# Performance work log

Measured on AMD Instinct MI355X. Metric: run time of the kernel, lower is better.

The kernel has to match this reference:

```python
import jax, jax.numpy as jnp
import numpy as np

WH, WW = 7, 7          # window size
S0, S1 = 3, 3          # shift size
NH = 12                # num heads
C = 384                # channels


def _rel_pos_index(wh, ww):
    coords = np.stack(np.meshgrid(np.arange(wh), np.arange(ww), indexing='ij')).reshape(2, -1)
    rel = coords[:, :, None] - coords[:, None, :]          # [2, N, N]
    rel = rel.transpose(1, 2, 0).astype(np.int64)          # [N, N, 2]
    rel[..., 0] += wh - 1
    rel[..., 1] += ww - 1
    rel[..., 0] *= 2 * ww - 1
    return rel.sum(-1)                                      # [N, N]


def _shift_mask(ph, pw, wh, ww, s0, s1):
    img = np.zeros((ph, pw), dtype=np.float32)
    cnt = 0
    for hs in ((0, ph - wh), (ph - wh, ph - s0), (ph - s0, ph)):
        for ws in ((0, pw - ww), (pw - ww, pw - s1), (pw - s1, pw)):
            img[hs[0]:hs[1], ws[0]:ws[1]] = cnt
            cnt += 1
    win = img.reshape(ph // wh, wh, pw // ww, ww).transpose(0, 2, 1, 3).reshape(-1, wh * ww)
    diff = win[:, None, :] - win[:, :, None]               # [nW, N, N]
    return np.where(diff != 0, -100.0, 0.0).astype(np.float32)


def setup_inputs() -> dict:
    key = jax.random.key(0)
    ks = jax.random.split(key, 6)
    return {
        'x': jax.random.normal(ks[0], (32, 56, 56, C), jnp.float32),
        'qkv_w': jax.random.normal(ks[1], (3 * C, C), jnp.float32) * 0.02,
        'qkv_b': jax.random.normal(ks[2], (3 * C,), jnp.float32) * 0.02,
        'proj_w': jax.random.normal(ks[3], (C, C), jnp.float32) * 0.02,
        'proj_b': jax.random.normal(ks[4], (C,), jnp.float32) * 0.02,
        'rpb_table': jax.random.normal(ks[5], ((2 * WH - 1) * (2 * WW - 1), NH), jnp.float32) * 0.02,
    }


def reference(x, qkv_w, qkv_b, proj_w, proj_b, rpb_table):
    b, h, w, c = x.shape
    pad_b, pad_r = (-h) % WH, (-w) % WW
    x = jnp.pad(x, ((0, 0), (0, pad_b), (0, pad_r), (0, 0)))
    ph, pw = h + pad_b, w + pad_r
    s0 = 0 if WH >= ph else S0
    s1 = 0 if WW >= pw else S1
    if s0 + s1 > 0:
        x = jnp.roll(x, (-s0, -s1), axis=(1, 2))
    nwh, nww = ph // WH, pw // WW
    nw = nwh * nww
    N = WH * WW
    hd = c // NH
    # window partition -> [b*nw, N, c]
    xw = x.reshape(b, nwh, WH, nww, WW, c).transpose(0, 1, 3, 2, 4, 5).reshape(b * nw, N, c)
    qkv = xw @ qkv_w.T + qkv_b
    qkv = qkv.reshape(b * nw, N, 3, NH, hd).transpose(2, 0, 3, 1, 4)  # [3, B_, H, N, hd]
    q, k, v = qkv[0] * (hd ** -0.5), qkv[1], qkv[2]
    attn = jnp.einsum('bhnd,bhmd->bhnm', q, k)                        # [B_, H, N, N]
    rel_idx = _rel_pos_index(WH, WW)
    bias = rpb_table[rel_idx.reshape(-1)].reshape(N, N, NH).transpose(2, 0, 1)
    attn = attn + bias[None]
    if s0 + s1 > 0:
        mask = jnp.asarray(_shift_mask(ph, pw, WH, WW, s0, s1))        # [nw, N, N]
        attn = attn.reshape(b, nw, NH, N, N) + mask[None, :, None]
        attn = attn.reshape(b * nw, NH, N, N)
    attn = jax.nn.softmax(attn, axis=-1)
    out = jnp.einsum('bhnm,bhmd->bhnd', attn, v).transpose(0, 2, 1, 3).reshape(b * nw, N, c)
    out = out @ proj_w.T + proj_b
    # window reverse -> [b, ph, pw, c]
    out = out.reshape(b, nwh, nww, WH, WW, c).transpose(0, 1, 3, 2, 4, 5).reshape(b, ph, pw, c)
    if s0 + s1 > 0:
        out = jnp.roll(out, (s0, s1), axis=(1, 2))
    return out[:, :h, :w, :]
```

## Files before the change

### kernel.cpp

```cpp
#include <hip/hip_runtime.h>
#include <hip/hip_bf16.h>
#include <stdint.h>


typedef __bf16 v8bf __attribute__((ext_vector_type(8)));
typedef __bf16 v4bf __attribute__((ext_vector_type(4)));
typedef float  v4f  __attribute__((ext_vector_type(4)));

#define MFMA16(a,b,c) __builtin_amdgcn_mfma_f32_16x16x32_bf16(a,b,c,0,0,0)

typedef const void __attribute__((address_space(1))) gas_t;
typedef void __attribute__((address_space(3))) las_t;

__device__ __forceinline__ void gl2lds16(const void* g, void* l) {
  __builtin_amdgcn_global_load_lds((gas_t*)g, (las_t*)l, 16, 0, 0);
}

__global__ __launch_bounds__(256) void gather_cvt_x(const float* __restrict__ x,
                                                    __bf16* __restrict__ xw) {
  uint32_t cid = blockIdx.x * 256u + threadIdx.x;
  uint32_t m   = cid / 96u, c4 = cid - (cid / 96u) * 96u;
  uint32_t win = m / 49u,  tok = m - win * 49u;
  uint32_t b  = win >> 6,  wy = (win >> 3) & 7u, wx = win & 7u;
  uint32_t ty = tok / 7u,  tx = tok - ty * 7u;
  uint32_t sy = wy * 7u + ty + 3u; if (sy >= 56u) sy -= 56u;
  uint32_t sx = wx * 7u + tx + 3u; if (sx >= 56u) sx -= 56u;
  const float4 v = *(const float4*)(x + (((size_t)(b * 56u + sy)) * 56u + sx) * 384u + c4 * 4u);
  v4bf o; o[0] = (__bf16)v.x; o[1] = (__bf16)v.y; o[2] = (__bf16)v.z; o[3] = (__bf16)v.w;
  *(v4bf*)(xw + (size_t)m * 384u + c4 * 4u) = o;
}

__global__ __launch_bounds__(256) void cvt_w_kernel(const float* __restrict__ qw,
                                                    const float* __restrict__ pw,
                                                    __bf16* __restrict__ dq,
                                                    __bf16* __restrict__ dp) {
  uint32_t cid = blockIdx.x * 256u + threadIdx.x;
  uint32_t e = cid * 4u;
  const float* src; __bf16* dst; uint32_t off;
  if (e < 442368u) { src = qw; dst = dq; off = e; }
  else             { src = pw; dst = dp; off = e - 442368u; }
  float4 v = *(const float4*)(src + off);
  v4bf o; o[0] = (__bf16)v.x; o[1] = (__bf16)v.y; o[2] = (__bf16)v.z; o[3] = (__bf16)v.w;
  *(v4bf*)(dst + off) = o;
}

template<int EPI>
__global__ __launch_bounds__(256) void gemm_bt(const __bf16* __restrict__ A,
                                               const __bf16* __restrict__ B,
                                               const float* __restrict__ biasv,
                                               __bf16* __restrict__ Qp,
                                               __bf16* __restrict__ Kp,
                                               __bf16* __restrict__ Vp,
                                               float* __restrict__ Op) {
  __shared__ __bf16 lds_a[128 * 32];
  __shared__ __bf16 lds_b[128 * 32];
  const int tid = threadIdx.x, wv = tid >> 6, ln = tid & 63;
  const int wr = wv >> 1, wc = wv & 1;
  const int c = ln & 15, rq = (ln >> 4) * 4;
  const uint32_t m0 = blockIdx.y * 128u, n0 = blockIdx.x * 128u;
  v4f acc[4][4] = {};
  for (int ks = 0; ks < 12; ++ks) {
    const uint32_t k0 = ks * 32u;
    for (int ch = wv; ch < 8; ch += 4) {
      uint32_t e = ch * 512u + (uint32_t)ln * 8u;
      uint32_t row = e >> 5, col = e & 31u;
      gl2lds16(A + (size_t)(m0 + row) * 384u + k0 + col, lds_a + ch * 512);
      gl2lds16(B + (size_t)(n0 + row) * 384u + k0 + col, lds_b + ch * 512);
    }
    __syncthreads();
    const __bf16* pa = lds_a + (wr * 64 + c) * 32 + rq * 2;
    const __bf16* pb = lds_b + (wc * 64 + c) * 32 + rq * 2;
    v8bf af[4], bfr[4];
#pragma unroll
    for (int i = 0; i < 4; ++i) af[i]  = *(const v8bf*)(pa + i * 16 * 32);
#pragma unroll
    for (int i = 0; i < 4; ++i) bfr[i] = *(const v8bf*)(pb + i * 16 * 32);
#pragma unroll
    for (int mi = 0; mi < 4; ++mi)
#pragma unroll
      for (int ni = 0; ni < 4; ++ni)
        acc[mi][ni] = MFMA16(af[mi], bfr[ni], acc[mi][ni]);
    __syncthreads();
  }

  if (EPI == 0) {
    const uint32_t which = blockIdx.x / 3u;
    __bf16* dst = (which == 0u) ? Qp : (which == 1u) ? Kp : Vp;
    const float scl = (which == 0u) ? 0.17677669529663687f : 1.0f;
#pragma unroll
    for (int ni = 0; ni < 4; ++ni) {
      uint32_t colg = n0 + wc * 64u + ni * 16u + c;
      float bv = biasv[colg];
      uint32_t cw = colg - which * 384u;
      uint32_t head = cw >> 5, d = cw & 31u;
#pragma unroll
      for (int mi = 0; mi < 4; ++mi)
#pragma unroll
        for (int r = 0; r < 4; ++r) {
          uint32_t mg = m0 + wr * 64u + mi * 16u + rq + r;
          uint32_t win = mg / 49u, tok = mg - win * 49u;
          float val = (acc[mi][ni][r] + bv) * scl;
          dst[((size_t)(win * 12u + head) * 49u + tok) * 32u + d] = (__bf16)val;
        }
    }
  } else {
#pragma unroll
    for (int ni = 0; ni < 4; ++ni) {
      uint32_t colg = n0 + wc * 64u + ni * 16u + c;
      float bv = biasv[colg];
#pragma unroll
      for (int mi = 0; mi < 4; ++mi)
#pragma unroll
        for (int r = 0; r < 4; ++r) {
          uint32_t mg = m0 + wr * 64u + mi * 16u + rq + r;
          uint32_t win = mg / 49u, tok = mg - win * 49u;
          uint32_t b = win >> 6, wy = (win >> 3) & 7u, wx = win & 7u;
          uint32_t ty = tok / 7u, tx = tok - ty * 7u;
          uint32_t y = wy * 7u + ty + 3u; if (y >= 56u) y -= 56u;
          uint32_t x = wx * 7u + tx + 3u; if (x >= 56u) x -= 56u;
          Op[(((size_t)b * 56u + y) * 56u + x) * 384u + colg] = acc[mi][ni][r] + bv;
        }
    }
  }
}

__global__ __launch_bounds__(256) void attn_kernel(const __bf16* __restrict__ Q,
                                                   const __bf16* __restrict__ K,
                                                   const __bf16* __restrict__ V,
                                                   const float* __restrict__ rpb,
                                                   __bf16* __restrict__ Oa) {
  __shared__ __bf16 plds[4][64 * 72];
  const int tid = threadIdx.x, wv = tid >> 6, ln = tid & 63;
  const int c = ln & 15, rq = (ln >> 4) * 4;
  const uint32_t gwh = blockIdx.x * 4u + wv;
  const uint32_t win = gwh / 12u, head = gwh - win * 12u;
  const uint32_t wy = (win >> 3) & 7u, wx = win & 7u;
  const __bf16* qb = Q + (size_t)gwh * 1568u;
  const __bf16* kb = K + (size_t)gwh * 1568u;
  const __bf16* vb = V + (size_t)gwh * 1568u;

  v8bf qf[4], kf[4];
#pragma unroll
  for (int t = 0; t < 4; ++t) {
    qf[t] = *(const v8bf*)(qb + (t * 16 + c) * 32 + rq * 2);
    kf[t] = *(const v8bf*)(kb + (t * 16 + c) * 32 + rq * 2);
  }
  v4f st[4][4] = {};
#pragma unroll
  for (int jt = 0; jt < 4; ++jt)
#pragma unroll
    for (int it = 0; it < 4; ++it)
      st[jt][it] = MFMA16(kf[jt], qf[it], st[jt][it]);

  int iy[4], ix[4], icls[4];
#pragma unroll
  for (int it = 0; it < 4; ++it) {
    int ii = it * 16 + c; if (ii > 48) ii = 48;
    int y = ii / 7, x = ii - y * 7;
    iy[it] = y; ix[it] = x;
    int cy = (wy == 7u) ? ((y < 4) ? 1 : 2) : 0;
    int cx = (wx == 7u) ? ((x < 4) ? 1 : 2) : 0;
    icls[it] = cy * 3 + cx;
  }
#pragma unroll
  for (int jt = 0; jt < 4; ++jt)
#pragma unroll
    for (int r = 0; r < 4; ++r) {
      int j = jt * 16 + rq + r;
      int jc = j > 48 ? 48 : j;
      int jy = jc / 7, jx = jc - jy * 7;
      int cy = (wy == 7u) ? ((jy < 4) ? 1 : 2) : 0;
      int cx = (wx == 7u) ? ((jx < 4) ? 1 : 2) : 0;
      int jcls = cy * 3 + cx;
      bool jvalid = (j < 49);
#pragma unroll
      for (int it = 0; it < 4; ++it) {
        float s = st[jt][it][r];
        if (jvalid) {
          int idx = ((iy[it] - jy + 6) * 13 + (ix[it] - jx + 6)) * 12 + (int)head;
          s += rpb[idx] + ((icls[it] == jcls) ? 0.f : -100.f);
        } else s = -1e30f;
        st[jt][it][r] = s;
      }
    }

  float rinv[4];
#pragma unroll
  for (int it = 0; it < 4; ++it) {
    float m = -1e30f;
#pragma unroll
    for (int jt = 0; jt < 4; ++jt)
#pragma unroll
      for (int r = 0; r < 4; ++r) m = fmaxf(m, st[jt][it][r]);
    m = fmaxf(m, __shfl_xor(m, 16));
    m = fmaxf(m, __shfl_xor(m, 32));
    float sum = 0.f;
#pragma unroll
    for (int jt = 0; jt < 4; ++jt)
#pragma unroll
      for (int r = 0; r < 4; ++r) {
        float p = __expf(st[jt][it][r] - m);
        st[jt][it][r] = p; sum += p;
      }
    sum += __shfl_xor(sum, 16);
    sum += __shfl_xor(sum, 32);
    rinv[it] = 1.0f / sum;
  }

  __bf16* pw = plds[wv];
#pragma unroll
  for (int jt = 0; jt < 4; ++jt)
#pragma unroll
    for (int it = 0; it < 4; ++it) {
      v4bf pk;
#pragma unroll
      for (int r = 0; r < 4; ++r) pk[r] = (__bf16)st[jt][it][r];
      *(v4bf*)(pw + (it * 16 + c) * 72 + jt * 16 + rq) = pk;
    }

  v4f ot[2][4] = {};
#pragma unroll
  for (int ks2 = 0; ks2 < 2; ++ks2) {
    v8bf av[2];
#pragma unroll
    for (int m16 = 0; m16 < 2; ++m16)
#pragma unroll
      for (int jj = 0; jj < 8; ++jj)
        av[m16][jj] = vb[(ks2 * 32 + rq * 2 + jj) * 32 + m16 * 16 + c];
#pragma unroll
    for (int it = 0; it < 4; ++it) {
      v8bf pf = *(const v8bf*)(pw + (it * 16 + c) * 72 + ks2 * 32 + rq * 2);
#pragma unroll
      for (int m16 = 0; m16 < 2; ++m16)
        ot[m16][it] = MFMA16(av[m16], pf, ot[m16][it]);
    }
  }

#pragma unroll
  for (int it = 0; it < 4; ++it) {
    int i = it * 16 + c;
    if (i < 49) {
      float ri = rinv[it];
#pragma unroll
      for (int m16 = 0; m16 < 2; ++m16) {
        v4bf o;
#pragma unroll
        for (int r = 0; r < 4; ++r) o[r] = (__bf16)(ot[m16][it][r] * ri);
        *(v4bf*)(Oa + ((size_t)win * 49u + i) * 384u + head * 32u + m16 * 16 + rq) = o;
      }
    }
  }
}

extern "C" void kernel_launch(void* const* d_in, const int* in_sizes, int n_in,
                              void* d_out, int out_size, void* d_ws, size_t ws_size,
                              hipStream_t stream) {
  const float* x      = (const float*)d_in[0];
  const float* qkv_w  = (const float*)d_in[1];
  const float* qkv_b  = (const float*)d_in[2];
  const float* proj_w = (const float*)d_in[3];
  const float* proj_b = (const float*)d_in[4];
  const float* rpb    = (const float*)d_in[5];
  float* out = (float*)d_out;

  char* w = (char*)d_ws;
  __bf16* Xw = (__bf16*)(w);
  __bf16* Wq = (__bf16*)(w + 77070336);
  __bf16* Wp = (__bf16*)(w + 77955072);
  __bf16* Qb = (__bf16*)(w + 78250240);
  __bf16* Kb = (__bf16*)(w + 78250240 + 77074432);
  __bf16* Vb = (__bf16*)(w + 78250240 + 154148864);

  gather_cvt_x<<<37632, 256, 0, stream>>>(x, Xw);
  cvt_w_kernel<<<576, 256, 0, stream>>>(qkv_w, proj_w, Wq, Wp);
  gemm_bt<0><<<dim3(9, 784), 256, 0, stream>>>(Xw, Wq, qkv_b, Qb, Kb, Vb, nullptr);
  attn_kernel<<<6144, 256, 0, stream>>>(Qb, Kb, Vb, rpb, Xw );
  gemm_bt<1><<<dim3(3, 784), 256, 0, stream>>>(Xw, Wp, proj_b, nullptr, nullptr, nullptr, out);
}
```

Measured before the change: 630.4 us.

## Fuse window gather and bf16 conversion into QKV GEMM; swizzle LDS, remap blocks

```diff
diff --git a/kernel.cpp b/kernel.cpp
--- a/kernel.cpp
+++ b/kernel.cpp
@@ -11,23 +11,8 @@
 
 typedef const void __attribute__((address_space(1))) gas_t;
 typedef void __attribute__((address_space(3))) las_t;
-
 __device__ __forceinline__ void gl2lds16(const void* g, void* l) {
   __builtin_amdgcn_global_load_lds((gas_t*)g, (las_t*)l, 16, 0, 0);
-}
-
-__global__ __launch_bounds__(256) void gather_cvt_x(const float* __restrict__ x,
-                                                    __bf16* __restrict__ xw) {
-  uint32_t cid = blockIdx.x * 256u + threadIdx.x;
-  uint32_t m   = cid / 96u, c4 = cid - (cid / 96u) * 96u;
-  uint32_t win = m / 49u,  tok = m - win * 49u;
-  uint32_t b  = win >> 6,  wy = (win >> 3) & 7u, wx = win & 7u;
-  uint32_t ty = tok / 7u,  tx = tok - ty * 7u;
-  uint32_t sy = wy * 7u + ty + 3u; if (sy >= 56u) sy -= 56u;
-  uint32_t sx = wx * 7u + tx + 3u; if (sx >= 56u) sx -= 56u;
-  const float4 v = *(const float4*)(x + (((size_t)(b * 56u + sy)) * 56u + sx) * 384u + c4 * 4u);
-  v4bf o; o[0] = (__bf16)v.x; o[1] = (__bf16)v.y; o[2] = (__bf16)v.z; o[3] = (__bf16)v.w;
-  *(v4bf*)(xw + (size_t)m * 384u + c4 * 4u) = o;
 }
 
 __global__ __launch_bounds__(256) void cvt_w_kernel(const float* __restrict__ qw,
@@ -45,63 +30,103 @@
 }
 
 template<int EPI>
-__global__ __launch_bounds__(256) void gemm_bt(const __bf16* __restrict__ A,
-                                               const __bf16* __restrict__ B,
+__global__ __launch_bounds__(256) void gemm_bt(const float* __restrict__ Xf,
+                                               const __bf16* __restrict__ Abf,
+                                               const __bf16* __restrict__ Bw,
                                                const float* __restrict__ biasv,
-                                               __bf16* __restrict__ Qp,
-                                               __bf16* __restrict__ Kp,
-                                               __bf16* __restrict__ Vp,
-                                               float* __restrict__ Op) {
-  __shared__ __bf16 lds_a[128 * 32];
-  __shared__ __bf16 lds_b[128 * 32];
+                                               __bf16* __restrict__ Cbf,
+                                               float* __restrict__ Of) {
+  constexpr uint32_t NT = (EPI == 0) ? 9u : 3u;
+  __shared__ __bf16 lds_a[128 * 64];
+  __shared__ __bf16 lds_b[128 * 64];
+  __shared__ uint32_t rowbase[128];
   const int tid = threadIdx.x, wv = tid >> 6, ln = tid & 63;
   const int wr = wv >> 1, wc = wv & 1;
   const int c = ln & 15, rq = (ln >> 4) * 4;
-  const uint32_t m0 = blockIdx.y * 128u, n0 = blockIdx.x * 128u;
+  const uint32_t chunk = gridDim.x >> 3;
+  const uint32_t phys = blockIdx.x;
+  const uint32_t lbid = (phys & 7u) * chunk + (phys >> 3);
+  const uint32_t mt = lbid / NT, nt = lbid - mt * NT;
+  const uint32_t m0 = mt * 128u, n0 = nt * 128u;
+
+  if (EPI == 0) {
+    if (tid < 128) {
+      uint32_t mg = m0 + tid;
+      uint32_t win = mg / 49u, tok = mg - win * 49u;
+      uint32_t b = win >> 6, wy = (win >> 3) & 7u, wx = win & 7u;
+      uint32_t ty = tok / 7u, tx = tok - ty * 7u;
+      uint32_t sy = wy * 7u + ty + 3u; if (sy >= 56u) sy -= 56u;
+      uint32_t sx = wx * 7u + tx + 3u; if (sx >= 56u) sx -= 56u;
+      rowbase[tid] = ((b * 56u + sy) * 56u + sx) * 384u;
+    }
+    __syncthreads();
+  }
+
   v4f acc[4][4] = {};
-  for (int ks = 0; ks < 12; ++ks) {
-    const uint32_t k0 = ks * 32u;
-    for (int ch = wv; ch < 8; ch += 4) {
-      uint32_t e = ch * 512u + (uint32_t)ln * 8u;
-      uint32_t row = e >> 5, col = e & 31u;
-      gl2lds16(A + (size_t)(m0 + row) * 384u + k0 + col, lds_a + ch * 512);
-      gl2lds16(B + (size_t)(n0 + row) * 384u + k0 + col, lds_b + ch * 512);
+  for (int ks = 0; ks < 6; ++ks) {
+    const uint32_t k0 = ks * 64u;
+#pragma unroll
+    for (int t = 0; t < 4; ++t) {
+      const int ch = wv + 4 * t;
+      uint32_t row = (uint32_t)ch * 8u + (uint32_t)(ln >> 3);
+      uint32_t u = ((uint32_t)(ln & 7)) ^ (row & 7u);
+      gl2lds16(Bw + (size_t)(n0 + row) * 384u + k0 + u * 8u, lds_b + ch * 512);
+      if (EPI == 1)
+        gl2lds16(Abf + (size_t)(m0 + row) * 384u + k0 + u * 8u, lds_a + ch * 512);
+    }
+    if (EPI == 0) {
+      const uint32_t arow = (uint32_t)(tid >> 4);
+      const uint32_t acol = (uint32_t)(tid & 15) * 4u;
+      float4 f[8];
+#pragma unroll
+      for (int p = 0; p < 8; ++p)
+        f[p] = *(const float4*)(Xf + rowbase[p * 16 + arow] + k0 + acol);
+#pragma unroll
+      for (int p = 0; p < 8; ++p) {
+        uint32_t row = (uint32_t)p * 16u + arow;
+        v4bf o; o[0] = (__bf16)f[p].x; o[1] = (__bf16)f[p].y;
+        o[2] = (__bf16)f[p].z; o[3] = (__bf16)f[p].w;
+        uint32_t byt = (row << 7) + ((acol * 2u) ^ ((row & 7u) << 4));
+        *(v4bf*)((char*)lds_a + byt) = o;
+      }
     }
     __syncthreads();
-    const __bf16* pa = lds_a + (wr * 64 + c) * 32 + rq * 2;
-    const __bf16* pb = lds_b + (wc * 64 + c) * 32 + rq * 2;
-    v8bf af[4], bfr[4];
-#pragma unroll
-    for (int i = 0; i < 4; ++i) af[i]  = *(const v8bf*)(pa + i * 16 * 32);
-#pragma unroll
-    for (int i = 0; i < 4; ++i) bfr[i] = *(const v8bf*)(pb + i * 16 * 32);
-#pragma unroll
-    for (int mi = 0; mi < 4; ++mi)
-#pragma unroll
-      for (int ni = 0; ni < 4; ++ni)
-        acc[mi][ni] = MFMA16(af[mi], bfr[ni], acc[mi][ni]);
+#pragma unroll
+    for (int kk = 0; kk < 2; ++kk) {
+      v8bf af[4], bfr[4];
+#pragma unroll
+      for (int mi = 0; mi < 4; ++mi) {
+        uint32_t row = (uint32_t)(wr * 64 + mi * 16 + c);
+        uint32_t byt = (row << 7) + (((uint32_t)(kk * 64 + rq * 4)) ^ ((row & 7u) << 4));
+        af[mi] = *(const v8bf*)((char*)lds_a + byt);
+      }
+#pragma unroll
+      for (int ni = 0; ni < 4; ++ni) {
+        uint32_t row = (uint32_t)(wc * 64 + ni * 16 + c);
+        uint32_t byt = (row << 7) + (((uint32_t)(kk * 64 + rq * 4)) ^ ((row & 7u) << 4));
+        bfr[ni] = *(const v8bf*)((char*)lds_b + byt);
+      }
+#pragma unroll
+      for (int mi = 0; mi < 4; ++mi)
+#pragma unroll
+        for (int ni = 0; ni < 4; ++ni)
+          acc[mi][ni] = MFMA16(af[mi], bfr[ni], acc[mi][ni]);
+    }
     __syncthreads();
   }
 
   if (EPI == 0) {
-    const uint32_t which = blockIdx.x / 3u;
-    __bf16* dst = (which == 0u) ? Qp : (which == 1u) ? Kp : Vp;
-    const float scl = (which == 0u) ? 0.17677669529663687f : 1.0f;
 #pragma unroll
     for (int ni = 0; ni < 4; ++ni) {
       uint32_t colg = n0 + wc * 64u + ni * 16u + c;
       float bv = biasv[colg];
-      uint32_t cw = colg - which * 384u;
-      uint32_t head = cw >> 5, d = cw & 31u;
-#pragma unroll
-      for (int mi = 0; mi < 4; ++mi)
-#pragma unroll
-        for (int r = 0; r < 4; ++r) {
-          uint32_t mg = m0 + wr * 64u + mi * 16u + rq + r;
-          uint32_t win = mg / 49u, tok = mg - win * 49u;
-          float val = (acc[mi][ni][r] + bv) * scl;
-          dst[((size_t)(win * 12u + head) * 49u + tok) * 32u + d] = (__bf16)val;
-        }
+#pragma unroll
+      for (int mi = 0; mi < 4; ++mi) {
+        uint32_t mg = m0 + wr * 64u + mi * 16u + rq;
+#pragma unroll
+        for (int r = 0; r < 4; ++r)
+          Cbf[(size_t)(mg + r) * 1152u + colg] = (__bf16)(acc[mi][ni][r] + bv);
+      }
     }
   } else {
 #pragma unroll
@@ -118,15 +143,13 @@
           uint32_t ty = tok / 7u, tx = tok - ty * 7u;
           uint32_t y = wy * 7u + ty + 3u; if (y >= 56u) y -= 56u;
           uint32_t x = wx * 7u + tx + 3u; if (x >= 56u) x -= 56u;
-          Op[(((size_t)b * 56u + y) * 56u + x) * 384u + colg] = acc[mi][ni][r] + bv;
+          Of[(((size_t)b * 56u + y) * 56u + x) * 384u + colg] = acc[mi][ni][r] + bv;
         }
     }
   }
 }
 
-__global__ __launch_bounds__(256) void attn_kernel(const __bf16* __restrict__ Q,
-                                                   const __bf16* __restrict__ K,
-                                                   const __bf16* __restrict__ V,
+__global__ __launch_bounds__(256) void attn_kernel(const __bf16* __restrict__ QKV,
                                                    const float* __restrict__ rpb,
                                                    __bf16* __restrict__ Oa) {
   __shared__ __bf16 plds[4][64 * 72];
@@ -135,15 +158,16 @@
   const uint32_t gwh = blockIdx.x * 4u + wv;
   const uint32_t win = gwh / 12u, head = gwh - win * 12u;
   const uint32_t wy = (win >> 3) & 7u, wx = win & 7u;
-  const __bf16* qb = Q + (size_t)gwh * 1568u;
-  const __bf16* kb = K + (size_t)gwh * 1568u;
-  const __bf16* vb = V + (size_t)gwh * 1568u;
+  const __bf16* qb = QKV + (size_t)win * 49u * 1152u + head * 32u;
+  const __bf16* kb = qb + 384;
+  const __bf16* vb = qb + 768;
 
   v8bf qf[4], kf[4];
 #pragma unroll
   for (int t = 0; t < 4; ++t) {
-    qf[t] = *(const v8bf*)(qb + (t * 16 + c) * 32 + rq * 2);
-    kf[t] = *(const v8bf*)(kb + (t * 16 + c) * 32 + rq * 2);
+    int rr = t * 16 + c; if (rr > 48) rr = 48;
+    qf[t] = *(const v8bf*)(qb + (size_t)rr * 1152u + rq * 2);
+    kf[t] = *(const v8bf*)(kb + (size_t)rr * 1152u + rq * 2);
   }
   v4f st[4][4] = {};
 #pragma unroll
@@ -152,6 +176,7 @@
     for (int it = 0; it < 4; ++it)
       st[jt][it] = MFMA16(kf[jt], qf[it], st[jt][it]);
 
+  const float scl = 0.17677669529663687f;
   int iy[4], ix[4], icls[4];
 #pragma unroll
   for (int it = 0; it < 4; ++it) {
@@ -178,7 +203,7 @@
         float s = st[jt][it][r];
         if (jvalid) {
           int idx = ((iy[it] - jy + 6) * 13 + (ix[it] - jx + 6)) * 12 + (int)head;
-          s += rpb[idx] + ((icls[it] == jcls) ? 0.f : -100.f);
+          s = s * scl + rpb[idx] + ((icls[it] == jcls) ? 0.f : -100.f);
         } else s = -1e30f;
         st[jt][it][r] = s;
       }
@@ -225,8 +250,10 @@
 #pragma unroll
     for (int m16 = 0; m16 < 2; ++m16)
 #pragma unroll
-      for (int jj = 0; jj < 8; ++jj)
-        av[m16][jj] = vb[(ks2 * 32 + rq * 2 + jj) * 32 + m16 * 16 + c];
+      for (int jj = 0; jj < 8; ++jj) {
+        int tok = ks2 * 32 + rq * 2 + jj; if (tok > 48) tok = 48;
+        av[m16][jj] = vb[(size_t)tok * 1152u + m16 * 16 + c];
+      }
 #pragma unroll
     for (int it = 0; it < 4; ++it) {
       v8bf pf = *(const v8bf*)(pw + (it * 16 + c) * 72 + ks2 * 32 + rq * 2);
@@ -264,16 +291,13 @@
   float* out = (float*)d_out;
 
   char* w = (char*)d_ws;
-  __bf16* Xw = (__bf16*)(w);
-  __bf16* Wq = (__bf16*)(w + 77070336);
-  __bf16* Wp = (__bf16*)(w + 77955072);
-  __bf16* Qb = (__bf16*)(w + 78250240);
-  __bf16* Kb = (__bf16*)(w + 78250240 + 77074432);
-  __bf16* Vb = (__bf16*)(w + 78250240 + 154148864);
-
-  gather_cvt_x<<<37632, 256, 0, stream>>>(x, Xw);
+  __bf16* Aout = (__bf16*)(w);
+  __bf16* Wq   = (__bf16*)(w + 77070336);
+  __bf16* Wp   = (__bf16*)(w + 77955072);
+  __bf16* QKV  = (__bf16*)(w + 78250240);
+
   cvt_w_kernel<<<576, 256, 0, stream>>>(qkv_w, proj_w, Wq, Wp);
-  gemm_bt<0><<<dim3(9, 784), 256, 0, stream>>>(Xw, Wq, qkv_b, Qb, Kb, Vb, nullptr);
-  attn_kernel<<<6144, 256, 0, stream>>>(Qb, Kb, Vb, rpb, Xw );
-  gemm_bt<1><<<dim3(3, 784), 256, 0, stream>>>(Xw, Wp, proj_b, nullptr, nullptr, nullptr, out);
-}
+  gemm_bt<0><<<7056, 256, 0, stream>>>(x, nullptr, Wq, qkv_b, QKV, nullptr);
+  attn_kernel<<<6144, 256, 0, stream>>>(QKV, rpb, Aout);
+  gemm_bt<1><<<2352, 256, 0, stream>>>(nullptr, Aout, Wp, proj_b, nullptr, out);
+}
```

Result: slower. 643.3 us (+2.0%).
